# Kernel tuning notes

Hardware: AMD Instinct MI355X
Metric: run time of the kernel (lower is better)

The kernel has to match this reference:

```python
import jax, jax.numpy as jnp
import numpy as np

B, L, D, H = 4, 1024, 768, 6
DH = D // H
EPS = 1e-5


def setup_inputs() -> dict:
    key = jax.random.key(0)
    kq, kk, kv, kl, kw = jax.random.split(key, 5)
    Q = jax.random.normal(kq, (B, L, D), jnp.float32)
    K = jax.random.normal(kk, (B, L, D), jnp.float32)
    V = jax.random.normal(kv, (B, L, D), jnp.float32)
    # realistic padding: each batch element has a valid length in [L//2, L]
    lengths = jax.random.randint(kl, (B,), L // 2, L + 1)
    valid = jnp.arange(L)[None, :] < lengths[:, None]          # (B, L)
    pad_mask = valid[:, :, None] & valid[:, None, :]           # (B, L, L), True = keep
    bx_packed = ~valid                                         # (B, L), True = padded
    # BatchNorm affine params (per-head channels)
    g1 = jnp.ones((H,), jnp.float32)
    b1 = jnp.zeros((H,), jnp.float32)
    g2 = jnp.ones((H,), jnp.float32)
    b2 = jnp.zeros((H,), jnp.float32)
    # posterior gate: Linear(H, 2)
    Wp = jax.random.normal(kw, (2, H), jnp.float32) * (1.0 / np.sqrt(H))
    bp = jnp.zeros((2,), jnp.float32)
    return {"Q": Q, "K": K, "V": V, "pad_mask": pad_mask, "bx_packed": bx_packed,
            "g1": g1, "b1": b1, "g2": g2, "b2": b2, "Wp": Wp, "bp": bp}


def _split_heads(x):
    b, l, _ = x.shape
    return x.reshape(b, l, H, DH).transpose(0, 2, 1, 3)  # (B, H, L, DH)


def _batchnorm(x, g, b):
    # x: (B, H, N); training-mode BatchNorm1d over channels H (stats over B and N)
    m = x.mean(axis=(0, 2), keepdims=True)
    v = x.var(axis=(0, 2), keepdims=True)  # biased, as torch uses for normalization
    return (x - m) * jax.lax.rsqrt(v + EPS) * g[None, :, None] + b[None, :, None]


def _remove_nan(x):
    return jnp.where(jnp.isnan(x), jnp.zeros_like(x), x)


def reference(Q, K, V, pad_mask, bx_packed, g1, b1, g2, b2, Wp, bp):
    Qh, Kh, Vh = _split_heads(Q), _split_heads(K), _split_heads(V)
    b, h, l, _ = Qh.shape
    # DistMatrix: negative squared Euclidean distance between query/key vectors
    # scores[b,h,i,j] = -||Q_i - K_j||^2, via the GEMM-friendly expansion
    q2 = jnp.sum(Qh * Qh, axis=-1)                     # (B, H, L)
    k2 = jnp.sum(Kh * Kh, axis=-1)                     # (B, H, L)
    qk = jnp.einsum("bhid,bhjd->bhij", Qh, Kh)         # (B, H, L, L)
    co = -(q2[..., :, None] + k2[..., None, :] - 2.0 * qk)
    # norm1 over flattened L*L
    co = _batchnorm(co.reshape(b, h, l * l), g1, b1).reshape(b, h, l, l)
    # zero out positions where pad_mask is False (in-place masked fill in torch)
    co = jnp.where(pad_mask[:, None, :, :], co, 0.0)
    co = jax.nn.softmax(co, axis=-1)
    co = _remove_nan(co)
    # column-sum attention mass per key position
    w = co.sum(axis=-2)                                # (B, H, L)
    w = _batchnorm(w, g2, b2).transpose(0, 2, 1)       # (B, L, H)
    # posterior gate: Linear(H,2) + softmax, take class-0 probability
    w = jax.nn.softmax(w @ Wp.T + bp, axis=-1)[..., 0]  # (B, L)
    w = _remove_nan(w)
    w = jnp.where(bx_packed, -jnp.inf, w)
    w = jax.nn.softmax(w, axis=-1)
    w = _remove_nan(w)[..., None]                      # (B, L, 1)
    return co, w, Vh
```

## Files before the change

kernel.cpp:

```cpp
#include <hip/hip_runtime.h>
#include <stdint.h>
#include <stddef.h>

#define BB 4
#define LL 1024
#define DD 768
#define HH 6
#define DHH 128
#define EPS 1e-5f
#define LOG2E 1.44269504088896f

#define CO_ELEMS 25165824
#define W_ELEMS  4096

#define OFF_Q2  0
#define OFF_K2  24576
#define OFF_WC  49152
#define OFF_SP  73728
#define OFF_AC  79872
#define OFF_SS  79888
#define OFF_WP  81920
#define OFF_GP  1654784
#define OFF_MS1 5193728
#define OFF_MS2 5242880
#define OFF_CT  5292032

typedef __attribute__((ext_vector_type(8))) short short8;
typedef __attribute__((ext_vector_type(4))) float f32x4;

__device__ __forceinline__ short8 ld_bf8(const float* __restrict__ p) {
    const float4 a = *(const float4*)(p);
    const float4 b = *(const float4*)(p + 4);
    short8 r;
    r[0] = (short)(__float_as_uint(a.x) >> 16);
    r[1] = (short)(__float_as_uint(a.y) >> 16);
    r[2] = (short)(__float_as_uint(a.z) >> 16);
    r[3] = (short)(__float_as_uint(a.w) >> 16);
    r[4] = (short)(__float_as_uint(b.x) >> 16);
    r[5] = (short)(__float_as_uint(b.y) >> 16);
    r[6] = (short)(__float_as_uint(b.z) >> 16);
    r[7] = (short)(__float_as_uint(b.w) >> 16);
    return r;
}

__device__ __forceinline__ short8 pack_bf8(float4 a, float4 b) {
    short8 r;
    r[0] = (short)(__float_as_uint(a.x) >> 16);
    r[1] = (short)(__float_as_uint(a.y) >> 16);
    r[2] = (short)(__float_as_uint(a.z) >> 16);
    r[3] = (short)(__float_as_uint(a.w) >> 16);
    r[4] = (short)(__float_as_uint(b.x) >> 16);
    r[5] = (short)(__float_as_uint(b.y) >> 16);
    r[6] = (short)(__float_as_uint(b.z) >> 16);
    r[7] = (short)(__float_as_uint(b.w) >> 16);
    return r;
}

__device__ __forceinline__ short8 pack_bf8v(f32x4 a, f32x4 b) {
    short8 r;
    r[0] = (short)(__float_as_uint(a[0]) >> 16);
    r[1] = (short)(__float_as_uint(a[1]) >> 16);
    r[2] = (short)(__float_as_uint(a[2]) >> 16);
    r[3] = (short)(__float_as_uint(a[3]) >> 16);
    r[4] = (short)(__float_as_uint(b[0]) >> 16);
    r[5] = (short)(__float_as_uint(b[1]) >> 16);
    r[6] = (short)(__float_as_uint(b[2]) >> 16);
    r[7] = (short)(__float_as_uint(b[3]) >> 16);
    return r;
}

__global__ __launch_bounds__(256) void k_gram(
        const float* __restrict__ Q, const float* __restrict__ K,
        const float* __restrict__ V,
        float* __restrict__ ws, float* __restrict__ gramP,
        float* __restrict__ ms1, float* __restrict__ ms2,
        float* __restrict__ vh, unsigned* __restrict__ ctr) {
    const int ic = blockIdx.x;
    const int bh = blockIdx.y;
    const int which = blockIdx.z;
    const int b = bh / HH, h = bh - b * HH;
    const int t = threadIdx.x;

    if (which == 2) {
        if (ic == 0 && bh == 0 && t < 32) ctr[t] = 0u;
        const float* srcv = V + (size_t)b * LL * DD + h * DHH;
        float* dstv = vh + ((size_t)bh * LL + (size_t)ic * 128) * DHH;
#pragma unroll
        for (int p = 0; p < 16; p++) {
            const int idx = p * 256 + t;
            const int row = idx >> 5, d4 = idx & 31;
            f32x4 v = *(const f32x4*)(srcv + (size_t)(ic * 128 + row) * DD + d4 * 4);
            __builtin_nontemporal_store(v, (f32x4*)(dstv + (size_t)row * DHH + d4 * 4));
        }
        return;
    }

    const float* src = (which ? K : Q) + (size_t)b * LL * DD + h * DHH;
    float* sqout = ws + (which ? OFF_K2 : OFF_Q2) + bh * 1024 + ic * 128;

    const int lane = t & 63, wv = t >> 6;
    const int lm = lane & 15, quad = lane >> 4;

    __shared__ float tileT[128][132];
    __shared__ float q2loc[128];

    const int ig = t >> 5;
    const int d0 = (t & 31) * 4;
#pragma unroll 4
    for (int p = 0; p < 16; p++) {
        const int i_loc = p * 8 + ig;
        float4 v = *(const float4*)(src + (size_t)(ic * 128 + i_loc) * DD + d0);
        tileT[d0 + 0][i_loc] = __uint_as_float(__float_as_uint(v.x) & 0xffff0000u);
        tileT[d0 + 1][i_loc] = __uint_as_float(__float_as_uint(v.y) & 0xffff0000u);
        tileT[d0 + 2][i_loc] = __uint_as_float(__float_as_uint(v.z) & 0xffff0000u);
        tileT[d0 + 3][i_loc] = __uint_as_float(__float_as_uint(v.w) & 0xffff0000u);
        float s = v.x * v.x + v.y * v.y + v.z * v.z + v.w * v.w;
#pragma unroll
        for (int off = 1; off < 32; off <<= 1) s += __shfl_xor(s, off);
        if ((t & 31) == 0) { q2loc[i_loc] = s; sqout[i_loc] = s; }
    }
    __syncthreads();

    if (t < 128) {
        float s1 = 0.f, s2 = 0.f;
#pragma unroll 8
        for (int i = 0; i < 128; i++) {
            float v = tileT[t][i];
            s1 += v;
            s2 += v * q2loc[i];
        }
        const size_t mo = ((size_t)(which * 24 + bh) * 8 + ic) * 128 + t;
        ms1[mo] = s1;
        ms2[mo] = s2;
    }

    const size_t gbase = ((size_t)(which * 24 + bh) * 8 + ic) * 9216;
    int pi = 0;
    for (int dt = 0; dt < 8; dt++) {
        for (int et = dt; et < 8; et++, pi++) {
            if ((pi & 3) != wv) continue;
            f32x4 acc = (f32x4)(0.0f);
#pragma unroll
            for (int kk = 0; kk < 4; kk++) {
                const int i0 = kk * 32 + quad * 8;
                const float* pa = &tileT[dt * 16 + lm][i0];
                const float* pb = &tileT[et * 16 + lm][i0];
                short8 af = pack_bf8v(*(const f32x4*)pa, *(const f32x4*)(pa + 4));
                short8 bf = pack_bf8v(*(const f32x4*)pb, *(const f32x4*)(pb + 4));
                acc = __builtin_amdgcn_mfma_f32_16x16x32_bf16(af, bf, acc, 0, 0, 0);
            }
            if (dt != et && which == 0) {
                acc[0] *= 2.f; acc[1] *= 2.f; acc[2] *= 2.f; acc[3] *= 2.f;
            }
            *(f32x4*)&gramP[gbase + (size_t)pi * 256 + lane * 4] = acc;
        }
    }
}

__global__ __launch_bounds__(1024) void k_stats3(
        const float* __restrict__ ms1, const float* __restrict__ ms2,
        const float* __restrict__ gramP,
        const float* __restrict__ q2, const float* __restrict__ k2,
        const float* __restrict__ g1, const float* __restrict__ b1,
        float* __restrict__ statsP, float* __restrict__ ac,
        unsigned* __restrict__ ctr) {
    const int bh = blockIdx.x;
    const int t = threadIdx.x, lane = t & 63, w = t >> 6;
    __shared__ float sQ[128], sK[128], sQq2[128], sKk2[128];
    __shared__ float sred[16][4];
    __shared__ float gred[16];

    if (t < 256) {
        const int d = t & 127, which = t >> 7;
        const float* p1 = ms1 + (size_t)(which * 24 + bh) * 1024 + d;
        const float* p2 = ms2 + (size_t)(which * 24 + bh) * 1024 + d;
        float s1 = 0.f, s2 = 0.f;
#pragma unroll
        for (int ic = 0; ic < 8; ic++) { s1 += p1[ic * 128]; s2 += p2[ic * 128]; }
        if (which) { sK[d] = s1; sKk2[d] = s2; }
        else       { sQ[d] = s1; sQq2[d] = s2; }
    }
    if (t >= 512 && t < 768) {
        const int tt = t - 512;
        f32x4 qv = *(const f32x4*)(q2 + bh * 1024 + tt * 4);
        f32x4 kv = *(const f32x4*)(k2 + bh * 1024 + tt * 4);
        float p0 = qv[0] + qv[1] + qv[2] + qv[3];
        float p1 = qv[0]*qv[0] + qv[1]*qv[1] + qv[2]*qv[2] + qv[3]*qv[3];
        float p2 = kv[0] + kv[1] + kv[2] + kv[3];
        float p3 = kv[0]*kv[0] + kv[1]*kv[1] + kv[2]*kv[2] + kv[3]*kv[3];
#pragma unroll
        for (int off = 1; off < 64; off <<= 1) {
            p0 += __shfl_xor(p0, off); p1 += __shfl_xor(p1, off);
            p2 += __shfl_xor(p2, off); p3 += __shfl_xor(p3, off);
        }
        if (lane == 0) { sred[w][0] = p0; sred[w][1] = p1; sred[w][2] = p2; sred[w][3] = p3; }
    }
    {
        const float* gq = gramP + (size_t)(0 * 24 + bh) * 8 * 9216;
        const float* gk = gramP + (size_t)(1 * 24 + bh) * 8 * 9216;
        float gg = 0.f;
#pragma unroll
        for (int it = 0; it < 9; it++) {
            const int f = it * 1024 + t;
            float a = 0.f, c = 0.f;
#pragma unroll
            for (int icc = 0; icc < 8; icc++) {
                a += gq[(size_t)icc * 9216 + f];
                c += gk[(size_t)icc * 9216 + f];
            }
            gg += a * c;
        }
#pragma unroll
        for (int off = 1; off < 64; off <<= 1) gg += __shfl_xor(gg, off);
        if (lane == 0) gred[w] = gg;
    }
    __syncthreads();
    if (t < 64) {
        float dA  = sQ[t] * sK[t] + sQ[t + 64] * sK[t + 64];
        float dBq = sQq2[t] * sK[t] + sQq2[t + 64] * sK[t + 64];
        float dBk = sQ[t] * sKk2[t] + sQ[t + 64] * sKk2[t + 64];
#pragma unroll
        for (int off = 1; off < 64; off <<= 1) {
            dA += __shfl_xor(dA, off); dBq += __shfl_xor(dBq, off); dBk += __shfl_xor(dBk, off);
        }
        if (t == 0) {
            float SQ2   = sred[8][0] + sred[9][0] + sred[10][0] + sred[11][0];
            float SQ2SQ = sred[8][1] + sred[9][1] + sred[10][1] + sred[11][1];
            float SK2   = sred[8][2] + sred[9][2] + sred[10][2] + sred[11][2];
            float SK2SQ = sred[8][3] + sred[9][3] + sred[10][3] + sred[11][3];
            float GG = 0.f;
#pragma unroll
            for (int i = 0; i < 16; i++) GG += gred[i];
            float sumS  = 2.f * dA - 1024.f * (SQ2 + SK2);
            float sumS2 = 4.f * GG + 1024.f * (SQ2SQ + SK2SQ) + 2.f * SQ2 * SK2 - 4.f * (dBq + dBk);
            statsP[bh * 2]     = sumS;
            statsP[bh * 2 + 1] = sumS2;
            __threadfence();
            unsigned old = atomicAdd(&ctr[30], 1u);
            if (old == 23u) {
                __threadfence();
#pragma unroll
                for (int h = 0; h < HH; h++) {
                    float T1 = 0.f, T2 = 0.f;
#pragma unroll
                    for (int b = 0; b < 4; b++) {
                        T1 += statsP[(b * HH + h) * 2];
                        T2 += statsP[(b * HH + h) * 2 + 1];
                    }
                    const float N = 4194304.f;
                    float m_ = T1 / N;
                    float var = fmaxf(T2 / N - m_ * m_, 0.0f);
                    float r = rsqrtf(var + EPS);
                    float a = r * g1[h];
                    ac[h] = a;
                    ac[8 + h] = b1[h] - m_ * a;
                }
            }
        }
    }
}

#define KLOAD(buf, jtv) do {                                                   \
    const float* _p = Kb + (size_t)(jw + (jtv) * 16 + lm) * DD + quad * 8;     \
    buf##0 = *(const float4*)(_p);        buf##1 = *(const float4*)(_p + 4);   \
    buf##2 = *(const float4*)(_p + 32);   buf##3 = *(const float4*)(_p + 36);  \
    buf##4 = *(const float4*)(_p + 64);   buf##5 = *(const float4*)(_p + 68);  \
    buf##6 = *(const float4*)(_p + 96);   buf##7 = *(const float4*)(_p + 100); \
} while (0)

#define KCOMP(buf, jtv) do {                                                   \
    short8 kf0 = pack_bf8(buf##0, buf##1);                                     \
    short8 kf1 = pack_bf8(buf##2, buf##3);                                     \
    short8 kf2 = pack_bf8(buf##4, buf##5);                                     \
    short8 kf3 = pack_bf8(buf##6, buf##7);                                     \
    f32x4 acc0 = (f32x4)(0.0f), acc1 = (f32x4)(0.0f);                          \
    acc0 = __builtin_amdgcn_mfma_f32_16x16x32_bf16(kf0, qf[0][0], acc0, 0, 0, 0); \
    acc1 = __builtin_amdgcn_mfma_f32_16x16x32_bf16(kf0, qf[1][0], acc1, 0, 0, 0); \
    acc0 = __builtin_amdgcn_mfma_f32_16x16x32_bf16(kf1, qf[0][1], acc0, 0, 0, 0); \
    acc1 = __builtin_amdgcn_mfma_f32_16x16x32_bf16(kf1, qf[1][1], acc1, 0, 0, 0); \
    acc0 = __builtin_amdgcn_mfma_f32_16x16x32_bf16(kf2, qf[0][2], acc0, 0, 0, 0); \
    acc1 = __builtin_amdgcn_mfma_f32_16x16x32_bf16(kf2, qf[1][2], acc1, 0, 0, 0); \
    acc0 = __builtin_amdgcn_mfma_f32_16x16x32_bf16(kf3, qf[0][3], acc0, 0, 0, 0); \
    acc1 = __builtin_amdgcn_mfma_f32_16x16x32_bf16(kf3, qf[1][3], acc1, 0, 0, 0); \
    const int jb = jw + (jtv) * 16;                                            \
    const f32x4 k2v = *(const f32x4*)(k2b + jb + quad * 4);                    \
    const uchar4 m4 = *(const uchar4*)(bxb + jb + quad * 4);                   \
    const bool vj0 = (m4.x == 0), vj1 = (m4.y == 0);                           \
    const bool vj2 = (m4.z == 0), vj3 = (m4.w == 0);                           \
    f32x4 kc;                                                                  \
    kc[0] = a1l * k2v[0]; kc[1] = a1l * k2v[1];                                \
    kc[2] = a1l * k2v[2]; kc[3] = a1l * k2v[3];                                \
    {                                                                          \
        f32x4 ev;                                                              \
        ev[0] = (vi0 && vj0) ? exp2f(fminf(fmaf(a2l, acc0[0], cr0 - kc[0]), 86.56f)) : 1.0f; \
        ev[1] = (vi0 && vj1) ? exp2f(fminf(fmaf(a2l, acc0[1], cr0 - kc[1]), 86.56f)) : 1.0f; \
        ev[2] = (vi0 && vj2) ? exp2f(fminf(fmaf(a2l, acc0[2], cr0 - kc[2]), 86.56f)) : 1.0f; \
        ev[3] = (vi0 && vj3) ? exp2f(fminf(fmaf(a2l, acc0[3], cr0 - kc[3]), 86.56f)) : 1.0f; \
        *(f32x4*)&e_lds[lm][jb + quad * 4] = ev;                               \
        rsum0 += (ev[0] + ev[1]) + (ev[2] + ev[3]);                            \
    }                                                                          \
    {                                                                          \
        f32x4 ev;                                                              \
        ev[0] = (vi1 && vj0) ? exp2f(fminf(fmaf(a2l, acc1[0], cr1 - kc[0]), 86.56f)) : 1.0f; \
        ev[1] = (vi1 && vj1) ? exp2f(fminf(fmaf(a2l, acc1[1], cr1 - kc[1]), 86.56f)) : 1.0f; \
        ev[2] = (vi1 && vj2) ? exp2f(fminf(fmaf(a2l, acc1[2], cr1 - kc[2]), 86.56f)) : 1.0f; \
        ev[3] = (vi1 && vj3) ? exp2f(fminf(fmaf(a2l, acc1[3], cr1 - kc[3]), 86.56f)) : 1.0f; \
        *(f32x4*)&e_lds[16 + lm][jb + quad * 4] = ev;                          \
        rsum1 += (ev[0] + ev[1]) + (ev[2] + ev[3]);                            \
    }                                                                          \
} while (0)

__global__ __launch_bounds__(512, 1) void k_fused(
        const float* __restrict__ Q, const float* __restrict__ Km,
        const float* __restrict__ q2, const float* __restrict__ k2,
        const float* __restrict__ ac, const unsigned char* __restrict__ bx,
        float* __restrict__ co, float* __restrict__ wcolP) {
    const int g = blockIdx.x;
    const int xcd = g & 7, slot = g >> 3;
    const int t = threadIdx.x, lane = t & 63, w = t >> 6;
    const int lm = lane & 15, quad = lane >> 4;
    const int jw = w * 128;

    __shared__ float e_lds[32][1028];
    __shared__ float rowsum[3][32];
    if (t < 96) ((float*)rowsum)[t] = 0.f;
    __syncthreads();

#pragma unroll 1
    for (int rep = 0; rep < 3; rep++) {
        const int idx = slot * 3 + rep;
        const int bh = xcd + ((idx >> 5) << 3);
        const int strip = idx & 31;
        const int b = bh / HH, h = bh - b * HH;
        const int i0 = strip * 32;
        const float* Qb = Q + (size_t)b * LL * DD + h * DHH;
        const float* Kb = Km + (size_t)b * LL * DD + h * DHH;
        const float* k2b = k2 + bh * 1024;
        const unsigned char* bxb = bx + b * LL;
        const float a1l = ac[h] * LOG2E;
        const float a2l = 2.0f * a1l;
        const float c1l = ac[8 + h] * LOG2E;

        short8 qf[2][4];
#pragma unroll
        for (int s = 0; s < 2; s++)
#pragma unroll
            for (int kk = 0; kk < 4; kk++)
                qf[s][kk] = ld_bf8(Qb + (size_t)(i0 + s * 16 + lm) * DD + kk * 32 + quad * 8);

        const bool vi0 = (bxb[i0 + lm] == 0);
        const bool vi1 = (bxb[i0 + 16 + lm] == 0);
        const float cr0 = c1l - a1l * q2[bh * 1024 + i0 + lm];
        const float cr1 = c1l - a1l * q2[bh * 1024 + i0 + 16 + lm];

        float4 rA0, rA1, rA2, rA3, rA4, rA5, rA6, rA7;
        float4 rB0, rB1, rB2, rB3, rB4, rB5, rB6, rB7;

        float rsum0 = 0.f, rsum1 = 0.f;
        KLOAD(rA, 0);
        KLOAD(rB, 1);
        KCOMP(rA, 0);
        KLOAD(rA, 2);
        KCOMP(rB, 1);
        KLOAD(rB, 3);
        KCOMP(rA, 2);
        KLOAD(rA, 4);
        KCOMP(rB, 3);
        KLOAD(rB, 5);
        KCOMP(rA, 4);
        KLOAD(rA, 6);
        KCOMP(rB, 5);
        KLOAD(rB, 7);
        KCOMP(rA, 6);
        KCOMP(rB, 7);

        rsum0 += __shfl_xor(rsum0, 16);
        rsum0 += __shfl_xor(rsum0, 32);
        rsum1 += __shfl_xor(rsum1, 16);
        rsum1 += __shfl_xor(rsum1, 32);
        if (lane < 16) {
            atomicAdd(&rowsum[rep][lm], rsum0);
            atomicAdd(&rowsum[rep][16 + lm], rsum1);
        }
        __syncthreads();

        const int cg = t & 255, rh = t >> 8;
        float* cob = co + ((size_t)bh << 20) + (size_t)(i0 + rh * 16) * 1024 + cg * 4;
        float* wp = wcolP + ((size_t)((strip * 2 + rh) * 24 + bh)) * 1024 + cg * 4;
        float cs0 = 0.f, cs1 = 0.f, cs2 = 0.f, cs3 = 0.f;
#pragma unroll
        for (int rr = 0; rr < 16; rr++) {
            const int r = rh * 16 + rr;
            const float inv = 1.0f / rowsum[rep][r];
            f32x4 v = *(const f32x4*)&e_lds[r][cg * 4];
            v[0] *= inv; v[1] *= inv; v[2] *= inv; v[3] *= inv;
            __builtin_nontemporal_store(v, (f32x4*)(cob + (size_t)rr * 1024));
            cs0 += v[0]; cs1 += v[1]; cs2 += v[2]; cs3 += v[3];
        }
        f32x4 wv; wv[0] = cs0; wv[1] = cs1; wv[2] = cs2; wv[3] = cs3;
        *(f32x4*)wp = wv;
        __syncthreads();
    }
}

__global__ __launch_bounds__(256) void k_wtail(
        const float* __restrict__ wcolP, float* __restrict__ wcol,
        float* __restrict__ ws2, unsigned* __restrict__ ctr,
        const unsigned char* __restrict__ bx,
        const float* __restrict__ g2, const float* __restrict__ b2,
        const float* __restrict__ Wp, const float* __restrict__ bp,
        float* __restrict__ wout) {
    const int t = threadIdx.x, lane = t & 63, w = t >> 6;
    __shared__ float sc[4][2];
    __shared__ int stail;
    __shared__ float abuf[12];

    const int g = blockIdx.x * 256 + t;
    float s = 0.f;
#pragma unroll 8
    for (int strip = 0; strip < 64; strip++)
        s += wcolP[(size_t)strip * 24576 + g];
    wcol[g] = s;
    float a = s, b = s * s;
#pragma unroll
    for (int off = 1; off < 64; off <<= 1) { a += __shfl_xor(a, off); b += __shfl_xor(b, off); }
    if (lane == 0) { sc[w][0] = a; sc[w][1] = b; }
    __syncthreads();
    if (t == 0) {
        ws2[blockIdx.x * 2]     = sc[0][0] + sc[1][0] + sc[2][0] + sc[3][0];
        ws2[blockIdx.x * 2 + 1] = sc[0][1] + sc[1][1] + sc[2][1] + sc[3][1];
    }
    asm volatile("s_waitcnt vmcnt(0)" ::: "memory");
    __threadfence();
    __syncthreads();
    if (t == 0) {
        unsigned o = atomicAdd(&ctr[25], 1u);
        stail = (o == 95u) ? 1 : 0;
    }
    __syncthreads();
    if (!stail) return;

    __threadfence();
    if (t < HH) {
        float ss = 0.f, ss2 = 0.f;
#pragma unroll
        for (int b_ = 0; b_ < 4; b_++) {
            const int bh = b_ * HH + t;
#pragma unroll
            for (int sub = 0; sub < 4; sub++) {
                const int blk = bh * 4 + sub;
                ss  += ws2[blk * 2];
                ss2 += ws2[blk * 2 + 1];
            }
        }
        float m = ss / 4096.f;
        float var = fmaxf(ss2 / 4096.f - m * m, 0.0f);
        float r = rsqrtf(var + EPS);
        float aa = r * g2[t];
        abuf[t] = aa;
        abuf[6 + t] = b2[t] - m * aa;
    }
    __syncthreads();
    if (w < 4) {
        const int b_ = w;
        const float bp0 = bp[0], bp1 = bp[1];
        float vbuf[16];
        float mx = -INFINITY;
#pragma unroll
        for (int u = 0; u < 16; u++) {
            const int l = lane * 16 + u;
            float z0 = bp0, z1 = bp1;
#pragma unroll
            for (int h_ = 0; h_ < HH; h_++) {
                const float wn = abuf[h_] * wcol[(b_ * HH + h_) * 1024 + l] + abuf[6 + h_];
                z0 += wn * Wp[h_];
                z1 += wn * Wp[HH + h_];
            }
            const float pc = 1.0f / (1.0f + __expf(z1 - z0));
            const float v_ = bx[b_ * LL + l] ? -INFINITY : pc;
            vbuf[u] = v_;
            mx = fmaxf(mx, v_);
        }
#pragma unroll
        for (int off = 1; off < 64; off <<= 1) mx = fmaxf(mx, __shfl_xor(mx, off));
        float ssum = 0.f;
#pragma unroll
        for (int u = 0; u < 16; u++) { vbuf[u] = __expf(vbuf[u] - mx); ssum += vbuf[u]; }
#pragma unroll
        for (int off = 1; off < 64; off <<= 1) ssum += __shfl_xor(ssum, off);
        const float inv_ = 1.0f / ssum;
#pragma unroll
        for (int u4 = 0; u4 < 4; u4++) {
            f32x4 o;
            o[0] = vbuf[u4 * 4 + 0] * inv_;
            o[1] = vbuf[u4 * 4 + 1] * inv_;
            o[2] = vbuf[u4 * 4 + 2] * inv_;
            o[3] = vbuf[u4 * 4 + 3] * inv_;
            *(f32x4*)&wout[b_ * 1024 + lane * 16 + u4 * 4] = o;
        }
    }
}

extern "C" void kernel_launch(void* const* d_in, const int* in_sizes, int n_in,
                              void* d_out, int out_size, void* d_ws, size_t ws_size,
                              hipStream_t stream) {
    const float* Q  = (const float*)d_in[0];
    const float* K  = (const float*)d_in[1];
    const float* V  = (const float*)d_in[2];
    const unsigned char* bx = (const unsigned char*)d_in[4];
    const float* g1 = (const float*)d_in[5];
    const float* b1 = (const float*)d_in[6];
    const float* g2 = (const float*)d_in[7];
    const float* b2 = (const float*)d_in[8];
    const float* Wp = (const float*)d_in[9];
    const float* bp = (const float*)d_in[10];

    float* out  = (float*)d_out;
    float* co   = out;
    float* wout = out + CO_ELEMS;
    float* vh   = out + CO_ELEMS + W_ELEMS;

    float* ws = (float*)d_ws;
    float* q2     = ws + OFF_Q2;
    float* k2     = ws + OFF_K2;
    float* wcol   = ws + OFF_WC;
    float* statsP = ws + OFF_SP;
    float* ac     = ws + OFF_AC;
    float* ws2    = ws + OFF_SS;
    float* wcolP  = ws + OFF_WP;
    float* gramP  = ws + OFF_GP;
    float* ms1    = ws + OFF_MS1;
    float* ms2    = ws + OFF_MS2;
    unsigned* ctr = (unsigned*)(ws + OFF_CT);

    k_gram<<<dim3(8, 24, 3), 256, 0, stream>>>(Q, K, V, ws, gramP, ms1, ms2, vh, ctr);
    k_stats3<<<24, 1024, 0, stream>>>(ms1, ms2, gramP, q2, k2, g1, b1, statsP, ac, ctr);
    k_fused<<<256, 512, 0, stream>>>(Q, K, q2, k2, ac, bx, co, wcolP);
    k_wtail<<<96, 256, 0, stream>>>(wcolP, wcol, ws2, ctr, bx, g2, b2, Wp, bp, wout);
}
```

Before: 272.6 us.

## Cache packed K fragments in registers across reps and allow two blocks per CU

The fused kernel now keeps all of a wave's K fragments, packed to bf16, in registers (kf[8][4]) and reloads them only when the batch-head changes between the three strip repetitions. The software double-buffered global loads of K are dropped. Launch bounds go from one to two blocks per CU, which lowers the per-thread register budget. The gram kernel's LDS tile padding drops from 132 to 129 and the vector LDS reads become scalar reads, so fewer registers are held there. The risks are register pressure or spills with 128 VGPRs of cached K plus Q fragments under the tighter budget, and lost load/compute overlap on the first rep.

```diff
diff --git a/kernel.cpp b/kernel.cpp
--- a/kernel.cpp
+++ b/kernel.cpp
@@ -56,19 +56,6 @@
     return r;
 }
 
-__device__ __forceinline__ short8 pack_bf8v(f32x4 a, f32x4 b) {
-    short8 r;
-    r[0] = (short)(__float_as_uint(a[0]) >> 16);
-    r[1] = (short)(__float_as_uint(a[1]) >> 16);
-    r[2] = (short)(__float_as_uint(a[2]) >> 16);
-    r[3] = (short)(__float_as_uint(a[3]) >> 16);
-    r[4] = (short)(__float_as_uint(b[0]) >> 16);
-    r[5] = (short)(__float_as_uint(b[1]) >> 16);
-    r[6] = (short)(__float_as_uint(b[2]) >> 16);
-    r[7] = (short)(__float_as_uint(b[3]) >> 16);
-    return r;
-}
-
 __global__ __launch_bounds__(256) void k_gram(
         const float* __restrict__ Q, const float* __restrict__ K,
         const float* __restrict__ V,
@@ -101,7 +88,7 @@
     const int lane = t & 63, wv = t >> 6;
     const int lm = lane & 15, quad = lane >> 4;
 
-    __shared__ float tileT[128][132];
+    __shared__ float tileT[128][129];
     __shared__ float q2loc[128];
 
     const int ig = t >> 5;
@@ -145,8 +132,12 @@
                 const int i0 = kk * 32 + quad * 8;
                 const float* pa = &tileT[dt * 16 + lm][i0];
                 const float* pb = &tileT[et * 16 + lm][i0];
-                short8 af = pack_bf8v(*(const f32x4*)pa, *(const f32x4*)(pa + 4));
-                short8 bf = pack_bf8v(*(const f32x4*)pb, *(const f32x4*)(pb + 4));
+                short8 af, bf;
+#pragma unroll
+                for (int e = 0; e < 8; e++) {
+                    af[e] = (short)(__float_as_uint(pa[e]) >> 16);
+                    bf[e] = (short)(__float_as_uint(pb[e]) >> 16);
+                }
                 acc = __builtin_amdgcn_mfma_f32_16x16x32_bf16(af, bf, acc, 0, 0, 0);
             }
             if (dt != et && which == 0) {
@@ -260,28 +251,24 @@
     }
 }
 
-#define KLOAD(buf, jtv) do {                                                   \
+#define KDIRECT(jtv) do {                                                      \
     const float* _p = Kb + (size_t)(jw + (jtv) * 16 + lm) * DD + quad * 8;     \
-    buf##0 = *(const float4*)(_p);        buf##1 = *(const float4*)(_p + 4);   \
-    buf##2 = *(const float4*)(_p + 32);   buf##3 = *(const float4*)(_p + 36);  \
-    buf##4 = *(const float4*)(_p + 64);   buf##5 = *(const float4*)(_p + 68);  \
-    buf##6 = *(const float4*)(_p + 96);   buf##7 = *(const float4*)(_p + 100); \
+    kf[jtv][0] = pack_bf8(*(const float4*)(_p),      *(const float4*)(_p + 4));   \
+    kf[jtv][1] = pack_bf8(*(const float4*)(_p + 32), *(const float4*)(_p + 36));  \
+    kf[jtv][2] = pack_bf8(*(const float4*)(_p + 64), *(const float4*)(_p + 68));  \
+    kf[jtv][3] = pack_bf8(*(const float4*)(_p + 96), *(const float4*)(_p + 100)); \
 } while (0)
 
-#define KCOMP(buf, jtv) do {                                                   \
-    short8 kf0 = pack_bf8(buf##0, buf##1);                                     \
-    short8 kf1 = pack_bf8(buf##2, buf##3);                                     \
-    short8 kf2 = pack_bf8(buf##4, buf##5);                                     \
-    short8 kf3 = pack_bf8(buf##6, buf##7);                                     \
+#define KCOMP2(jtv) do {                                                       \
     f32x4 acc0 = (f32x4)(0.0f), acc1 = (f32x4)(0.0f);                          \
-    acc0 = __builtin_amdgcn_mfma_f32_16x16x32_bf16(kf0, qf[0][0], acc0, 0, 0, 0); \
-    acc1 = __builtin_amdgcn_mfma_f32_16x16x32_bf16(kf0, qf[1][0], acc1, 0, 0, 0); \
-    acc0 = __builtin_amdgcn_mfma_f32_16x16x32_bf16(kf1, qf[0][1], acc0, 0, 0, 0); \
-    acc1 = __builtin_amdgcn_mfma_f32_16x16x32_bf16(kf1, qf[1][1], acc1, 0, 0, 0); \
-    acc0 = __builtin_amdgcn_mfma_f32_16x16x32_bf16(kf2, qf[0][2], acc0, 0, 0, 0); \
-    acc1 = __builtin_amdgcn_mfma_f32_16x16x32_bf16(kf2, qf[1][2], acc1, 0, 0, 0); \
-    acc0 = __builtin_amdgcn_mfma_f32_16x16x32_bf16(kf3, qf[0][3], acc0, 0, 0, 0); \
-    acc1 = __builtin_amdgcn_mfma_f32_16x16x32_bf16(kf3, qf[1][3], acc1, 0, 0, 0); \
+    acc0 = __builtin_amdgcn_mfma_f32_16x16x32_bf16(kf[jtv][0], qf[0][0], acc0, 0, 0, 0); \
+    acc1 = __builtin_amdgcn_mfma_f32_16x16x32_bf16(kf[jtv][0], qf[1][0], acc1, 0, 0, 0); \
+    acc0 = __builtin_amdgcn_mfma_f32_16x16x32_bf16(kf[jtv][1], qf[0][1], acc0, 0, 0, 0); \
+    acc1 = __builtin_amdgcn_mfma_f32_16x16x32_bf16(kf[jtv][1], qf[1][1], acc1, 0, 0, 0); \
+    acc0 = __builtin_amdgcn_mfma_f32_16x16x32_bf16(kf[jtv][2], qf[0][2], acc0, 0, 0, 0); \
+    acc1 = __builtin_amdgcn_mfma_f32_16x16x32_bf16(kf[jtv][2], qf[1][2], acc1, 0, 0, 0); \
+    acc0 = __builtin_amdgcn_mfma_f32_16x16x32_bf16(kf[jtv][3], qf[0][3], acc0, 0, 0, 0); \
+    acc1 = __builtin_amdgcn_mfma_f32_16x16x32_bf16(kf[jtv][3], qf[1][3], acc1, 0, 0, 0); \
     const int jb = jw + (jtv) * 16;                                            \
     const f32x4 k2v = *(const f32x4*)(k2b + jb + quad * 4);                    \
     const uchar4 m4 = *(const uchar4*)(bxb + jb + quad * 4);                   \
@@ -310,7 +297,7 @@
     }                                                                          \
 } while (0)
 
-__global__ __launch_bounds__(512, 1) void k_fused(
+__global__ __launch_bounds__(512, 2) void k_fused(
         const float* __restrict__ Q, const float* __restrict__ Km,
         const float* __restrict__ q2, const float* __restrict__ k2,
         const float* __restrict__ ac, const unsigned char* __restrict__ bx,
@@ -326,6 +313,9 @@
     if (t < 96) ((float*)rowsum)[t] = 0.f;
     __syncthreads();
 
+    short8 kf[8][4];
+    int cached_bh = -1;
+
 #pragma unroll 1
     for (int rep = 0; rep < 3; rep++) {
         const int idx = slot * 3 + rep;
@@ -334,13 +324,19 @@
         const int b = bh / HH, h = bh - b * HH;
         const int i0 = strip * 32;
         const float* Qb = Q + (size_t)b * LL * DD + h * DHH;
-        const float* Kb = Km + (size_t)b * LL * DD + h * DHH;
         const float* k2b = k2 + bh * 1024;
         const unsigned char* bxb = bx + b * LL;
         const float a1l = ac[h] * LOG2E;
         const float a2l = 2.0f * a1l;
         const float c1l = ac[8 + h] * LOG2E;
 
+        if (bh != cached_bh) {
+            cached_bh = bh;
+            const float* Kb = Km + (size_t)b * LL * DD + h * DHH;
+            KDIRECT(0); KDIRECT(1); KDIRECT(2); KDIRECT(3);
+            KDIRECT(4); KDIRECT(5); KDIRECT(6); KDIRECT(7);
+        }
+
         short8 qf[2][4];
 #pragma unroll
         for (int s = 0; s < 2; s++)
@@ -353,26 +349,9 @@
         const float cr0 = c1l - a1l * q2[bh * 1024 + i0 + lm];
         const float cr1 = c1l - a1l * q2[bh * 1024 + i0 + 16 + lm];
 
-        float4 rA0, rA1, rA2, rA3, rA4, rA5, rA6, rA7;
-        float4 rB0, rB1, rB2, rB3, rB4, rB5, rB6, rB7;
-
         float rsum0 = 0.f, rsum1 = 0.f;
-        KLOAD(rA, 0);
-        KLOAD(rB, 1);
-        KCOMP(rA, 0);
-        KLOAD(rA, 2);
-        KCOMP(rB, 1);
-        KLOAD(rB, 3);
-        KCOMP(rA, 2);
-        KLOAD(rA, 4);
-        KCOMP(rB, 3);
-        KLOAD(rB, 5);
-        KCOMP(rA, 4);
-        KLOAD(rA, 6);
-        KCOMP(rB, 5);
-        KLOAD(rB, 7);
-        KCOMP(rA, 6);
-        KCOMP(rB, 7);
+        KCOMP2(0); KCOMP2(1); KCOMP2(2); KCOMP2(3);
+        KCOMP2(4); KCOMP2(5); KCOMP2(6); KCOMP2(7);
 
         rsum0 += __shfl_xor(rsum0, 16);
         rsum0 += __shfl_xor(rsum0, 32);
```

Measured after the change: 267.3 us. About the same (-1.9%).
